# Optimization experiments

Measured on AMD Instinct MI355X. Metric: run time of the kernel, lower is better.

Reference implementation:

```python
import jax, jax.numpy as jnp
import numpy as np

OBJ_VD = 4096  # obj_config['visual_d']


def _forward3(x, Wh, bh, We, be):
    # HypernymVisual_acc.forward3 (dropout is identity in eval)
    x = jax.nn.relu(x)
    h = jax.nn.relu(x @ Wh.T + bh)
    return h @ We.T + be


def _po_sim(hypers, hypos):
    # PartialOrderSimilarity with p=2: -||relu(hypers - hypos)||_2 over last axis
    d = jax.nn.relu(hypers - hypos)
    return -jnp.sqrt(jnp.sum(d * d, axis=-1))


def setup_inputs() -> dict:
    key = jax.random.key(0)
    ks = jax.random.split(key, 18)
    B, NNEG, V, ED = 1024, 128, 100, 600
    s = 0.02
    return {
        "vfs": jax.random.normal(ks[0], (B, 12288), jnp.float32),
        "label_vecs": jax.random.normal(ks[1], (V, ED), jnp.float32),
        "pls": jax.random.randint(ks[2], (B,), 0, V),
        "nls": jax.random.randint(ks[3], (B, NNEG), 0, V),
        "W_h1": jax.random.normal(ks[4], (2048, 4096), jnp.float32) * s,
        "b_h1": jax.random.normal(ks[5], (2048,), jnp.float32) * s,
        "W_e1": jax.random.normal(ks[6], (600, 2048), jnp.float32) * s,
        "b_e1": jax.random.normal(ks[7], (600,), jnp.float32) * s,
        "W_h2": jax.random.normal(ks[8], (4096, 12288), jnp.float32) * s,
        "b_h2": jax.random.normal(ks[9], (4096,), jnp.float32) * s,
        "W_e2": jax.random.normal(ks[10], (600, 4096), jnp.float32) * s,
        "b_e2": jax.random.normal(ks[11], (600,), jnp.float32) * s,
        "W_h": jax.random.normal(ks[12], (1800, 1800), jnp.float32) * s,
        "b_h": jax.random.normal(ks[13], (1800,), jnp.float32) * s,
        "W_e": jax.random.normal(ks[14], (600, 1800), jnp.float32) * s,
        "b_e": jax.random.normal(ks[15], (600,), jnp.float32) * s,
    }


def reference(vfs, label_vecs, pls, nls,
              W_h1, b_h1, W_e1, b_e1,
              W_h2, b_h2, W_e2, b_e2,
              W_h, b_h, W_e, b_e):
    # PredicateVisual_acc.forward1 (dropout as eval identity)
    sbj = _forward3(vfs[:, :OBJ_VD], W_h1, b_h1, W_e1, b_e1)   # [B, 600]
    obj = _forward3(vfs[:, -OBJ_VD:], W_h1, b_h1, W_e1, b_e1)  # [B, 600]
    pre = _forward3(vfs, W_h2, b_h2, W_e2, b_e2)               # [B, 600]
    z = jnp.concatenate([sbj, pre, obj], axis=1)               # [B, 1800]
    z = jax.nn.relu(z)
    h = jax.nn.relu(z @ W_h.T + b_h)                           # [B, 1800]
    emb = h @ W_e.T + b_e                                      # [B, 600]
    p_scores = _po_sim(label_vecs[pls], emb)                   # [B]
    n_scores = _po_sim(label_vecs[nls], emb[:, None, :])       # [B, NNEG]
    return jnp.concatenate([p_scores[:, None], n_scores], axis=1)
```

## Files before the change

### kernel.cpp

```cpp
#include <hip/hip_runtime.h>
#include <hip/hip_bf16.h>

using f32x4  = __attribute__((ext_vector_type(4))) float;
using bf16x8 = __attribute__((ext_vector_type(8))) __bf16;

typedef const __attribute__((address_space(1))) unsigned int GU32;
typedef __attribute__((address_space(3))) unsigned int LU32;

__device__ __forceinline__ void gload_lds16(void* l, const void* g) {
    __builtin_amdgcn_global_load_lds((GU32*)g, (LU32*)l, 16, 0, 0);
}

template <int RELU, int BF16OUT, int PARTIAL>
__global__ __launch_bounds__(256)
void gemm_bf16(const __bf16* __restrict__ A, int lda, long long a2_off, int msplit,
               const __bf16* __restrict__ Wt, int ldw, int wrows,
               const float* __restrict__ bias,
               void* __restrict__ Cout, int ldc, long long c2_off,
               int N, int K, int kchunk)
{
    __shared__ bf16x8 As[1024];
    __shared__ bf16x8 Ws[1024];

    const int t  = threadIdx.x;
    const int l  = t & 63;
    const int w  = t >> 6;
    const int m0 = blockIdx.y << 7;
    const int n0 = blockIdx.x << 7;
    const int kb0 = blockIdx.z * kchunk;
    const int ke  = min(kb0 + kchunk, K);

    const __bf16* Ab = A + ((m0 >= msplit) ? a2_off : 0);

    const __bf16* asrc[4];
    const __bf16* wsrc[4];
    int dslot[4];
#pragma unroll
    for (int it = 0; it < 4; ++it) {
        int slot = w * 256 + it * 64 + l;
        int kg   = slot >> 7;
        int row  = slot & 127;
        asrc[it] = Ab + (size_t)(m0 + row) * lda + kg * 8 + kb0;
        int wrow = n0 + row; if (wrow >= wrows) wrow = wrows - 1;
        wsrc[it] = Wt + (size_t)wrow * ldw + kg * 8 + kb0;
        dslot[it] = w * 256 + it * 64;
    }

    const int lr = l & 15, lkg = l >> 4;
    const int wr = (w >> 1) << 6, wc = (w & 1) << 6;

    f32x4 acc[4][4] = {};

    for (int kb = kb0; kb < ke; kb += 64) {
#pragma unroll
        for (int it = 0; it < 4; ++it) {
            gload_lds16(&As[dslot[it]], asrc[it]);
            gload_lds16(&Ws[dslot[it]], wsrc[it]);
            asrc[it] += 64; wsrc[it] += 64;
        }
        __syncthreads();
#pragma unroll
        for (int ks = 0; ks < 2; ++ks) {
            const int kgf = ks * 4 + lkg;
            bf16x8 af[4], wf[4];
#pragma unroll
            for (int m = 0; m < 4; ++m) af[m] = As[kgf * 128 + wr + m * 16 + lr];
#pragma unroll
            for (int n = 0; n < 4; ++n) wf[n] = Ws[kgf * 128 + wc + n * 16 + lr];
#pragma unroll
            for (int m = 0; m < 4; ++m)
#pragma unroll
                for (int n = 0; n < 4; ++n)
                    acc[m][n] = __builtin_amdgcn_mfma_f32_16x16x32_bf16(
                        af[m], wf[n], acc[m][n], 0, 0, 0);
        }
        __syncthreads();
    }

    const long long coff = PARTIAL ? (long long)blockIdx.z * c2_off
                                   : ((m0 >= msplit) ? c2_off : 0);
#pragma unroll
    for (int n = 0; n < 4; ++n) {
        int col = n0 + wc + n * 16 + lr;
        if (col >= N) continue;
        float bv = PARTIAL ? 0.f : bias[col];
#pragma unroll
        for (int m = 0; m < 4; ++m) {
            int rbase = m0 + wr + m * 16 + lkg * 4;
#pragma unroll
            for (int j = 0; j < 4; ++j) {
                long long idx = (long long)(rbase + j) * ldc + col + coff;
                if (PARTIAL) {
                    ((float*)Cout)[idx] = acc[m][n][j];
                } else {
                    float v = acc[m][n][j] + bv;
                    if (RELU) v = fmaxf(v, 0.f);
                    if (BF16OUT) ((__bf16*)Cout)[idx] = (__bf16)v;
                    else         ((float*)Cout)[idx]  = v;
                }
            }
        }
    }
}

template <int RELU, int BF16OUT>
__global__ __launch_bounds__(256)
void reduce_k(const float* __restrict__ part, long long zs, int S,
              const float* __restrict__ bias, void* __restrict__ out,
              int N, int ldc, int msplit, long long c2, int M)
{
    const int n8 = N >> 3;
    const long long total = (long long)M * n8;
    for (long long i = (long long)blockIdx.x * 256 + threadIdx.x; i < total;
         i += (long long)gridDim.x * 256) {
        int row = (int)(i / n8);
        int c8  = (int)(i - (long long)row * n8) << 3;
        long long base = (long long)row * N + c8;
        float4 s0 = {0.f, 0.f, 0.f, 0.f}, s1 = {0.f, 0.f, 0.f, 0.f};
        for (int s = 0; s < S; ++s) {
            const float4* p = (const float4*)(part + s * zs + base);
            float4 a = p[0], b = p[1];
            s0.x += a.x; s0.y += a.y; s0.z += a.z; s0.w += a.w;
            s1.x += b.x; s1.y += b.y; s1.z += b.z; s1.w += b.w;
        }
        float v[8] = {s0.x, s0.y, s0.z, s0.w, s1.x, s1.y, s1.z, s1.w};
        long long ob = (long long)row * ldc + c8 + ((row >= msplit) ? c2 : 0);
        if (BF16OUT) {
            bf16x8 o;
#pragma unroll
            for (int j = 0; j < 8; ++j) {
                float x = v[j] + bias[c8 + j];
                if (RELU) x = fmaxf(x, 0.f);
                o[j] = (__bf16)x;
            }
            *(bf16x8*)((__bf16*)out + ob) = o;
        } else {
            float4 o0, o1;
            float t0[8];
#pragma unroll
            for (int j = 0; j < 8; ++j) {
                float x = v[j] + bias[c8 + j];
                if (RELU) x = fmaxf(x, 0.f);
                t0[j] = x;
            }
            o0 = {t0[0], t0[1], t0[2], t0[3]};
            o1 = {t0[4], t0[5], t0[6], t0[7]};
            *(float4*)((float*)out + ob)     = o0;
            *(float4*)((float*)out + ob + 4) = o1;
        }
    }
}

__global__ __launch_bounds__(256)
void conv_bf16(const float* __restrict__ in, __bf16* __restrict__ out,
               long long n, int relu)
{
    long long stride = (long long)gridDim.x * 256 * 8;
    for (long long i = ((long long)blockIdx.x * 256 + threadIdx.x) * 8; i < n; i += stride) {
        float4 f0 = *(const float4*)(in + i);
        float4 f1 = *(const float4*)(in + i + 4);
        float v[8] = {f0.x, f0.y, f0.z, f0.w, f1.x, f1.y, f1.z, f1.w};
        bf16x8 o;
#pragma unroll
        for (int j = 0; j < 8; ++j) {
            float x = v[j];
            if (relu) x = fmaxf(x, 0.f);
            o[j] = (__bf16)x;
        }
        *(bf16x8*)(out + i) = o;
    }
}

__global__ __launch_bounds__(256)
void conv_pad(const float* __restrict__ in, __bf16* __restrict__ out,
              int rows, int cols, int ldo)
{
    int v8 = ldo >> 3;
    long long total = (long long)rows * v8;
    for (long long s = (long long)blockIdx.x * 256 + threadIdx.x; s < total;
         s += (long long)gridDim.x * 256) {
        int r  = (int)(s / v8);
        int c8 = ((int)(s % v8)) << 3;
        bf16x8 o;
        if (c8 + 8 <= cols) {
            const float* p = in + (size_t)r * cols + c8;
            float4 f0 = *(const float4*)p;
            float4 f1 = *(const float4*)(p + 4);
            float v[8] = {f0.x, f0.y, f0.z, f0.w, f1.x, f1.y, f1.z, f1.w};
#pragma unroll
            for (int j = 0; j < 8; ++j) o[j] = (__bf16)v[j];
        } else {
#pragma unroll
            for (int j = 0; j < 8; ++j) o[j] = (__bf16)0.f;
        }
        *(bf16x8*)(out + (size_t)r * ldo + c8) = o;
    }
}

__global__ __launch_bounds__(256)
void zero_cols(__bf16* __restrict__ buf, int rows, int c0, int ld)
{
    int wpad = ld - c0;
    int total = rows * wpad;
    for (int i = blockIdx.x * 256 + threadIdx.x; i < total; i += gridDim.x * 256)
        buf[(size_t)(i / wpad) * ld + c0 + (i % wpad)] = (__bf16)0.f;
}

__global__ __launch_bounds__(256)
void score_kernel(const float* __restrict__ emb,
                  const float* __restrict__ labels,
                  const int* __restrict__ pls,
                  const int* __restrict__ nls,
                  float* __restrict__ out)
{
    const int b = blockIdx.x;
    __shared__ float e[600];
    for (int i = threadIdx.x; i < 600; i += 256) e[i] = emb[(size_t)b * 600 + i];
    __syncthreads();

    const int w = threadIdx.x >> 6;
    const int lane = threadIdx.x & 63;
    for (int j = w; j < 129; j += 4) {
        int idx = (j == 0) ? pls[b] : nls[(size_t)b * 128 + (j - 1)];
        const float* lv = labels + (size_t)idx * 600;
        float s = 0.f;
        for (int d = lane; d < 600; d += 64) {
            float df = lv[d] - e[d];
            df = fmaxf(df, 0.f);
            s += df * df;
        }
#pragma unroll
        for (int off = 32; off >= 1; off >>= 1) s += __shfl_xor(s, off, 64);
        if (lane == 0) out[(size_t)b * 129 + j] = -sqrtf(s);
    }
}

extern "C" void kernel_launch(void* const* d_in, const int* in_sizes, int n_in,
                              void* d_out, int out_size, void* d_ws, size_t ws_size,
                              hipStream_t stream)
{
    const float* vfs    = (const float*)d_in[0];
    const float* labels = (const float*)d_in[1];
    const int*   pls    = (const int*)d_in[2];
    const int*   nls    = (const int*)d_in[3];
    const float* W_h1   = (const float*)d_in[4];
    const float* b_h1   = (const float*)d_in[5];
    const float* W_e1   = (const float*)d_in[6];
    const float* b_e1   = (const float*)d_in[7];
    const float* W_h2   = (const float*)d_in[8];
    const float* b_h2   = (const float*)d_in[9];
    const float* W_e2   = (const float*)d_in[10];
    const float* b_e2   = (const float*)d_in[11];
    const float* W_h    = (const float*)d_in[12];
    const float* b_h    = (const float*)d_in[13];
    const float* W_e    = (const float*)d_in[14];
    const float* b_e    = (const float*)d_in[15];

    char* p = (char*)d_ws;
    auto alloc = [&](size_t bytes) { char* r = p; p += (bytes + 255) & ~size_t(255); return r; };
    __bf16* vfs_bf = (__bf16*)alloc(1024ll * 12288 * 2);
    __bf16* h1     = (__bf16*)alloc(2048ll * 2048 * 2);
    __bf16* hp     = (__bf16*)alloc(1024ll * 4096 * 2);
    __bf16* z      = (__bf16*)alloc(1024ll * 1856 * 2);
    __bf16* h2     = (__bf16*)alloc(1024ll * 1856 * 2);
    float*  emb    = (float*)alloc(1024ll * 600 * 4);
    __bf16* Wh1b   = (__bf16*)alloc(2048ll * 4096 * 2);
    __bf16* Wh2b   = (__bf16*)alloc(4096ll * 12288 * 2);
    __bf16* We1b   = (__bf16*)alloc(600ll * 2048 * 2);
    __bf16* We2b   = (__bf16*)alloc(600ll * 4096 * 2);
    __bf16* Whb    = (__bf16*)alloc(1800ll * 1856 * 2);
    __bf16* Web    = (__bf16*)alloc(600ll * 1856 * 2);

    size_t used  = (size_t)(p - (char*)d_ws);
    size_t rem   = (ws_size > used) ? (ws_size - used) : 0;
    size_t arena = rem > (64u << 20) ? (64u << 20) : (rem & ~size_t(255));
    float* part  = (float*)alloc(arena);

    dim3 blk(256);
    const int HUGE_SPLIT = 1 << 30;

    auto pickS = [&](int M, int N, int smax) {
        int s = smax;
        while (s > 1 && (long long)s * M * N * 4 > (long long)arena) s >>= 1;
        return s;
    };
    auto gemm = [&](const __bf16* A, int lda, long long a2, int msA,
                    const __bf16* W, int ldw, int wrows, const float* bias,
                    void* out, int ldc, int msC, long long c2,
                    int M, int N, int K, int relu, int bf16out, int smax) {
        int S = pickS(M, N, smax);
        int nx = (N + 127) >> 7, ny = M >> 7;
        if (S == 1) {
            if (bf16out)
                gemm_bf16<1, 1, 0><<<dim3(nx, ny, 1), blk, 0, stream>>>(
                    A, lda, a2, (msA == HUGE_SPLIT ? msC : msA), W, ldw, wrows,
                    bias, out, ldc, c2, N, K, K);
            else
                gemm_bf16<0, 0, 0><<<dim3(nx, ny, 1), blk, 0, stream>>>(
                    A, lda, a2, (msA == HUGE_SPLIT ? msC : msA), W, ldw, wrows,
                    bias, out, ldc, c2, N, K, K);
        } else {
            int kchunk = (((K + S - 1) / S) + 63) & ~63;
            long long zs = (long long)M * N;
            gemm_bf16<0, 0, 1><<<dim3(nx, ny, S), blk, 0, stream>>>(
                A, lda, a2, msA, W, ldw, wrows, nullptr,
                part, N, zs, N, K, kchunk);
            long long tot8 = (long long)M * (N >> 3);
            int rblocks = (int)((tot8 + 255) / 256);
            if (rblocks > 2048) rblocks = 2048;
            if (bf16out)
                reduce_k<1, 1><<<dim3(rblocks), blk, 0, stream>>>(
                    part, zs, S, bias, out, N, ldc, msC, c2, M);
            else
                reduce_k<0, 0><<<dim3(rblocks), blk, 0, stream>>>(
                    part, zs, S, bias, out, N, ldc, msC, c2, M);
        }
    };

    conv_bf16<<<2048, blk, 0, stream>>>(vfs, vfs_bf, 1024ll * 12288, 1);
    conv_bf16<<<1024, blk, 0, stream>>>(W_h1, Wh1b, 2048ll * 4096, 0);
    conv_bf16<<<2048, blk, 0, stream>>>(W_h2, Wh2b, 4096ll * 12288, 0);
    conv_bf16<<<512,  blk, 0, stream>>>(W_e1, We1b, 600ll * 2048, 0);
    conv_bf16<<<512,  blk, 0, stream>>>(W_e2, We2b, 600ll * 4096, 0);
    conv_pad<<<1024, blk, 0, stream>>>(W_h, Whb, 1800, 1800, 1856);
    conv_pad<<<512,  blk, 0, stream>>>(W_e, Web, 600, 1800, 1856);
    zero_cols<<<256, blk, 0, stream>>>(z,  1024, 1800, 1856);
    zero_cols<<<256, blk, 0, stream>>>(h2, 1024, 1800, 1856);

    gemm(vfs_bf, 12288, 8192ll - 1024ll * 12288, 1024,
         Wh1b, 4096, 2048, b_h1, h1, 2048, HUGE_SPLIT, 0,
         2048, 2048, 4096, 1, 1, 4);
    gemm(vfs_bf, 12288, 0, HUGE_SPLIT,
         Wh2b, 12288, 4096, b_h2, hp, 4096, HUGE_SPLIT, 0,
         1024, 4096, 12288, 1, 1, 4);
    gemm(h1, 2048, 0, HUGE_SPLIT,
         We1b, 2048, 600, b_e1, z, 1856, 1024, 1200ll - 1024ll * 1856,
         2048, 600, 2048, 1, 1, 8);
    gemm(hp, 4096, 0, HUGE_SPLIT,
         We2b, 4096, 600, b_e2, z + 600, 1856, HUGE_SPLIT, 0,
         1024, 600, 4096, 1, 1, 8);
    gemm(z, 1856, 0, HUGE_SPLIT,
         Whb, 1856, 1800, b_h, h2, 1856, HUGE_SPLIT, 0,
         1024, 1800, 1856, 1, 1, 4);
    gemm(h2, 1856, 0, HUGE_SPLIT,
         Web, 1856, 600, b_e, emb, 600, HUGE_SPLIT, 0,
         1024, 600, 1856, 0, 0, 8);

    score_kernel<<<dim3(1024), blk, 0, stream>>>(emb, labels, pls, nls, (float*)d_out);
}
```

Baseline: 936.2 us.

## Use 64x64-tile GEMMs for small layers and fuse the two embedding GEMMs

Refactors the GEMM into a templated body with a selectable tile size. The four small GEMMs (the two embedding projections, the fusion hidden layer and the final embedding) now use 64x64 tiles without split-K, so the partial-sum buffer writes and the reduce kernels go away. The two independent embedding GEMMs (h1 and hp projections into z) are merged into one launch by picking a descriptor per block index. The cost is longer per-block K loops with less data reuse per tile, and less parallelism than the split-K version had.

```diff
diff --git a/kernel.cpp b/kernel.cpp
--- a/kernel.cpp
+++ b/kernel.cpp
@@ -11,49 +11,42 @@
     __builtin_amdgcn_global_load_lds((GU32*)g, (LU32*)l, 16, 0, 0);
 }
 
-template <int RELU, int BF16OUT, int PARTIAL>
-__global__ __launch_bounds__(256)
-void gemm_bf16(const __bf16* __restrict__ A, int lda, long long a2_off, int msplit,
-               const __bf16* __restrict__ Wt, int ldw, int wrows,
-               const float* __restrict__ bias,
-               void* __restrict__ Cout, int ldc, long long c2_off,
-               int N, int K, int kchunk)
-{
-    __shared__ bf16x8 As[1024];
-    __shared__ bf16x8 Ws[1024];
-
-    const int t  = threadIdx.x;
-    const int l  = t & 63;
-    const int w  = t >> 6;
-    const int m0 = blockIdx.y << 7;
-    const int n0 = blockIdx.x << 7;
-    const int kb0 = blockIdx.z * kchunk;
-    const int ke  = min(kb0 + kchunk, K);
+template <int TM, int RELU, int BF16OUT, int PARTIAL>
+__device__ __forceinline__ void gemm_body(
+    bf16x8* As, bf16x8* Ws,
+    const __bf16* __restrict__ A, int lda, long long a2_off, int msplit,
+    const __bf16* __restrict__ Wt, int ldw, int wrows,
+    const float* __restrict__ bias,
+    void* __restrict__ Cout, int ldc, long long c2_off,
+    int N, int K, int m0, int n0, int kb0, int ke, int zslice)
+{
+    constexpr int NIT = TM / 32;
+    constexpr int FR  = TM / 32;
+    const int t = threadIdx.x, l = t & 63, w = t >> 6;
 
     const __bf16* Ab = A + ((m0 >= msplit) ? a2_off : 0);
-
-    const __bf16* asrc[4];
-    const __bf16* wsrc[4];
-    int dslot[4];
-#pragma unroll
-    for (int it = 0; it < 4; ++it) {
-        int slot = w * 256 + it * 64 + l;
-        int kg   = slot >> 7;
-        int row  = slot & 127;
+    const __bf16* asrc[NIT];
+    const __bf16* wsrc[NIT];
+    int dslot[NIT];
+#pragma unroll
+    for (int it = 0; it < NIT; ++it) {
+        int slot = (w * NIT + it) * 64 + l;
+        int kg   = slot / TM;
+        int row  = slot % TM;
         asrc[it] = Ab + (size_t)(m0 + row) * lda + kg * 8 + kb0;
         int wrow = n0 + row; if (wrow >= wrows) wrow = wrows - 1;
         wsrc[it] = Wt + (size_t)wrow * ldw + kg * 8 + kb0;
-        dslot[it] = w * 256 + it * 64;
+        dslot[it] = (w * NIT + it) * 64;
     }
 
     const int lr = l & 15, lkg = l >> 4;
-    const int wr = (w >> 1) << 6, wc = (w & 1) << 6;
-
-    f32x4 acc[4][4] = {};
+    const int wr = (w >> 1) * (TM / 2), wc = (w & 1) * (TM / 2);
+
+    f32x4 acc[FR][FR] = {};
 
     for (int kb = kb0; kb < ke; kb += 64) {
 #pragma unroll
-        for (int it = 0; it < 4; ++it) {
+        for (int it = 0; it < NIT; ++it) {
             gload_lds16(&As[dslot[it]], asrc[it]);
             gload_lds16(&Ws[dslot[it]], wsrc[it]);
             asrc[it] += 64; wsrc[it] += 64;
@@ -62,30 +55,30 @@
 #pragma unroll
         for (int ks = 0; ks < 2; ++ks) {
             const int kgf = ks * 4 + lkg;
-            bf16x8 af[4], wf[4];
-#pragma unroll
-            for (int m = 0; m < 4; ++m) af[m] = As[kgf * 128 + wr + m * 16 + lr];
-#pragma unroll
-            for (int n = 0; n < 4; ++n) wf[n] = Ws[kgf * 128 + wc + n * 16 + lr];
-#pragma unroll
-            for (int m = 0; m < 4; ++m)
-#pragma unroll
-                for (int n = 0; n < 4; ++n)
+            bf16x8 af[FR], wf[FR];
+#pragma unroll
+            for (int m = 0; m < FR; ++m) af[m] = As[kgf * TM + wr + m * 16 + lr];
+#pragma unroll
+            for (int n = 0; n < FR; ++n) wf[n] = Ws[kgf * TM + wc + n * 16 + lr];
+#pragma unroll
+            for (int m = 0; m < FR; ++m)
+#pragma unroll
+                for (int n = 0; n < FR; ++n)
                     acc[m][n] = __builtin_amdgcn_mfma_f32_16x16x32_bf16(
                         af[m], wf[n], acc[m][n], 0, 0, 0);
         }
         __syncthreads();
     }
 
-    const long long coff = PARTIAL ? (long long)blockIdx.z * c2_off
+    const long long coff = PARTIAL ? (long long)zslice * c2_off
                                    : ((m0 >= msplit) ? c2_off : 0);
 #pragma unroll
-    for (int n = 0; n < 4; ++n) {
+    for (int n = 0; n < FR; ++n) {
         int col = n0 + wc + n * 16 + lr;
         if (col >= N) continue;
         float bv = PARTIAL ? 0.f : bias[col];
 #pragma unroll
-        for (int m = 0; m < 4; ++m) {
+        for (int m = 0; m < FR; ++m) {
             int rbase = m0 + wr + m * 16 + lkg * 4;
 #pragma unroll
             for (int j = 0; j < 4; ++j) {
@@ -101,6 +94,45 @@
             }
         }
     }
+}
+
+template <int RELU, int BF16OUT, int PARTIAL>
+__global__ __launch_bounds__(256)
+void gemm128(const __bf16* __restrict__ A, int lda, long long a2_off, int msplit,
+             const __bf16* __restrict__ Wt, int ldw, int wrows,
+             const float* __restrict__ bias,
+             void* __restrict__ Cout, int ldc, long long c2_off,
+             int N, int K, int kchunk)
+{
+    __shared__ bf16x8 As[1024];
+    __shared__ bf16x8 Ws[1024];
+    int kb0 = blockIdx.z * kchunk;
+    int ke  = min(kb0 + kchunk, K);
+    gemm_body<128, RELU, BF16OUT, PARTIAL>(
+        As, Ws, A, lda, a2_off, msplit, Wt, ldw, wrows, bias,
+        Cout, ldc, c2_off, N, K, blockIdx.y << 7, blockIdx.x << 7,
+        kb0, ke, blockIdx.z);
+}
+
+struct GDesc {
+    const __bf16* A; const __bf16* W; const float* bias; void* out;
+    long long a2, c2;
+    int lda, ldw, wrows, ldc, N, K, ntx, msplit;
+};
+
+template <int RELU, int BF16OUT>
+__global__ __launch_bounds__(256)
+void gemm64_dual(GDesc d0, GDesc d1, int nblk0)
+{
+    __shared__ bf16x8 As[512];
+    __shared__ bf16x8 Ws[512];
+    int bid = blockIdx.x;
+    GDesc d = (bid < nblk0) ? d0 : d1;
+    int tid = (bid < nblk0) ? bid : bid - nblk0;
+    int tx = tid % d.ntx, ty = tid / d.ntx;
+    gemm_body<64, RELU, BF16OUT, 0>(
+        As, Ws, d.A, d.lda, d.a2, d.msplit, d.W, d.ldw, d.wrows, d.bias,
+        d.out, d.ldc, d.c2, d.N, d.K, ty << 6, tx << 6, 0, d.K, 0);
 }
 
 template <int RELU, int BF16OUT>
@@ -135,7 +167,6 @@
             }
             *(bf16x8*)((__bf16*)out + ob) = o;
         } else {
-            float4 o0, o1;
             float t0[8];
 #pragma unroll
             for (int j = 0; j < 8; ++j) {
@@ -143,8 +174,8 @@
                 if (RELU) x = fmaxf(x, 0.f);
                 t0[j] = x;
             }
-            o0 = {t0[0], t0[1], t0[2], t0[3]};
-            o1 = {t0[4], t0[5], t0[6], t0[7]};
+            float4 o0 = {t0[0], t0[1], t0[2], t0[3]};
+            float4 o1 = {t0[4], t0[5], t0[6], t0[7]};
             *(float4*)((float*)out + ob)     = o0;
             *(float4*)((float*)out + ob + 4) = o1;
         }
@@ -287,33 +318,24 @@
     auto gemm = [&](const __bf16* A, int lda, long long a2, int msA,
                     const __bf16* W, int ldw, int wrows, const float* bias,
                     void* out, int ldc, int msC, long long c2,
-                    int M, int N, int K, int relu, int bf16out, int smax) {
+                    int M, int N, int K, int smax) {
         int S = pickS(M, N, smax);
         int nx = (N + 127) >> 7, ny = M >> 7;
         if (S == 1) {
-            if (bf16out)
-                gemm_bf16<1, 1, 0><<<dim3(nx, ny, 1), blk, 0, stream>>>(
-                    A, lda, a2, (msA == HUGE_SPLIT ? msC : msA), W, ldw, wrows,
-                    bias, out, ldc, c2, N, K, K);
-            else
-                gemm_bf16<0, 0, 0><<<dim3(nx, ny, 1), blk, 0, stream>>>(
-                    A, lda, a2, (msA == HUGE_SPLIT ? msC : msA), W, ldw, wrows,
-                    bias, out, ldc, c2, N, K, K);
+            gemm128<1, 1, 0><<<dim3(nx, ny, 1), blk, 0, stream>>>(
+                A, lda, a2, (msA == HUGE_SPLIT ? msC : msA), W, ldw, wrows,
+                bias, out, ldc, c2, N, K, K);
         } else {
             int kchunk = (((K + S - 1) / S) + 63) & ~63;
             long long zs = (long long)M * N;
-            gemm_bf16<0, 0, 1><<<dim3(nx, ny, S), blk, 0, stream>>>(
+            gemm128<0, 0, 1><<<dim3(nx, ny, S), blk, 0, stream>>>(
                 A, lda, a2, msA, W, ldw, wrows, nullptr,
                 part, N, zs, N, K, kchunk);
             long long tot8 = (long long)M * (N >> 3);
             int rblocks = (int)((tot8 + 255) / 256);
             if (rblocks > 2048) rblocks = 2048;
-            if (bf16out)
-                reduce_k<1, 1><<<dim3(rblocks), blk, 0, stream>>>(
-                    part, zs, S, bias, out, N, ldc, msC, c2, M);
-            else
-                reduce_k<0, 0><<<dim3(rblocks), blk, 0, stream>>>(
-                    part, zs, S, bias, out, N, ldc, msC, c2, M);
+            reduce_k<1, 1><<<dim3(rblocks), blk, 0, stream>>>(
+                part, zs, S, bias, out, N, ldc, msC, c2, M);
         }
     };
 
@@ -329,22 +351,28 @@
 
     gemm(vfs_bf, 12288, 8192ll - 1024ll * 12288, 1024,
          Wh1b, 4096, 2048, b_h1, h1, 2048, HUGE_SPLIT, 0,
-         2048, 2048, 4096, 1, 1, 4);
+         2048, 2048, 4096, 4);
     gemm(vfs_bf, 12288, 0, HUGE_SPLIT,
          Wh2b, 12288, 4096, b_h2, hp, 4096, HUGE_SPLIT, 0,
-         1024, 4096, 12288, 1, 1, 4);
-    gemm(h1, 2048, 0, HUGE_SPLIT,
-         We1b, 2048, 600, b_e1, z, 1856, 1024, 1200ll - 1024ll * 1856,
-         2048, 600, 2048, 1, 1, 8);
-    gemm(hp, 4096, 0, HUGE_SPLIT,
-         We2b, 4096, 600, b_e2, z + 600, 1856, HUGE_SPLIT, 0,
-         1024, 600, 4096, 1, 1, 8);
-    gemm(z, 1856, 0, HUGE_SPLIT,
-         Whb, 1856, 1800, b_h, h2, 1856, HUGE_SPLIT, 0,
-         1024, 1800, 1856, 1, 1, 4);
-    gemm(h2, 1856, 0, HUGE_SPLIT,
-         Web, 1856, 600, b_e, emb, 600, HUGE_SPLIT, 0,
-         1024, 600, 1856, 0, 0, 8);
+         1024, 4096, 12288, 4);
+
+    {
+        GDesc d3{h1,  We1b, b_e1, z,       0, 1200ll - 1024ll * 1856,
+                 2048, 2048, 600, 1856, 600, 2048, 10, 1024};
+        GDesc d4{hp,  We2b, b_e2, z + 600, 0, 0,
+                 4096, 4096, 600, 1856, 600, 4096, 10, HUGE_SPLIT};
+        gemm64_dual<1, 1><<<dim3(480), blk, 0, stream>>>(d3, d4, 320);
+    }
+    {
+        GDesc d5{z, Whb, b_h, h2, 0, 0,
+                 1856, 1856, 1800, 1856, 1800, 1856, 29, HUGE_SPLIT};
+        gemm64_dual<1, 1><<<dim3(464), blk, 0, stream>>>(d5, d5, 464);
+    }
+    {
+        GDesc d6{h2, Web, b_e, emb, 0, 0,
+                 1856, 1856, 600, 600, 600, 1856, 10, HUGE_SPLIT};
+        gemm64_dual<0, 0><<<dim3(160), blk, 0, stream>>>(d6, d6, 160);
+    }
 
     score_kernel<<<dim3(1024), blk, 0, stream>>>(emb, labels, pls, nls, (float*)d_out);
 }
```

Measured after the change: 952.2 us. About the same (+1.7%).
